# Optimization experiments

Measured on AMD Instinct MI355X. Metric: run time of the kernel, lower is better.

Reference implementation:

```python
import jax, jax.numpy as jnp
import numpy as np

B, L, D, H = 4, 1024, 1024, 16
HD = D // H            # head_dim = 64
MAX_LEN = 1024         # pos_max_len
SCALE = HD ** 0.5


def setup_inputs() -> dict:
    key = jax.random.key(0)
    ks = jax.random.split(key, 7)
    sd = 1.0 / np.sqrt(D)
    x = jax.random.normal(ks[0], (B, L, D), dtype=jnp.float32)
    Wq = jax.random.normal(ks[1], (D, D), dtype=jnp.float32) * sd
    Wk = jax.random.normal(ks[2], (D, D), dtype=jnp.float32) * sd
    Wv = jax.random.normal(ks[3], (D, D), dtype=jnp.float32) * sd
    Wo = jax.random.normal(ks[4], (D, D), dtype=jnp.float32) * sd
    # relative positional embedding tables [2*max_len+1, head_dim]
    pek = jax.random.normal(ks[5], (2 * MAX_LEN + 1, HD), dtype=jnp.float32) / np.sqrt(HD)
    pev = jax.random.normal(ks[6], (2 * MAX_LEN + 1, HD), dtype=jnp.float32) / np.sqrt(HD)
    return {"x": x, "Wq": Wq, "Wk": Wk, "Wv": Wv, "Wo": Wo, "pek": pek, "pev": pev}


def _rel_idx(seq_len):
    r = jnp.arange(seq_len)
    dist = r[None, :] - r[:, None]                 # k - q, [L, L]
    return jnp.clip(dist, -MAX_LEN, MAX_LEN) + MAX_LEN


def reference(x, Wq, Wk, Wv, Wo, pek, pev):
    b, s, _ = x.shape
    # projections (nn.Linear: x @ W.T), split heads -> [b, h, s, d]
    def proj(W):
        return (x @ W.T).reshape(b, s, H, HD).transpose(0, 2, 1, 3)
    Q, K, V = proj(Wq), proj(Wk), proj(Wv)

    scores = jnp.einsum('bhqd,bhkd->bhqk', Q, K) / SCALE
    idx = _rel_idx(s)                              # [s, s]
    rel_k = pek[idx]                               # [s, s, hd]
    scores = scores + jnp.einsum('bhqd,qkd->bhqk', Q, rel_k) / SCALE

    causal = jnp.tril(jnp.ones((s, s), dtype=bool))
    scores = jnp.where(causal[None, None], scores, -jnp.inf)
    attn = jax.nn.softmax(scores, axis=-1)         # [b, h, q, k]

    out = jnp.einsum('bhqk,bhkd->bhqd', attn, V)
    rel_v = pev[idx]                               # [s, s, hd]
    out = out + jnp.einsum('bhqk,qkd->bhqd', attn, rel_v)

    out = out.transpose(0, 2, 1, 3).reshape(b, s, D)
    return out @ Wo.T
```

## Files before the change

### kernel.cpp

```cpp
#include <hip/hip_runtime.h>
#include <hip/hip_bf16.h>

typedef __hip_bfloat16 bf16;
using bfv8 = __attribute__((ext_vector_type(8))) __bf16;
using f4_t = __attribute__((ext_vector_type(4))) float;

#define DEVI static __device__ __forceinline__

DEVI unsigned short f2bu(float f) {
    bf16 h = __float2bfloat16(f);
    return __builtin_bit_cast(unsigned short, h);
}
DEVI ushort4 f4_to_b4(float4 v) {
    ushort4 r;
    r.x = f2bu(v.x); r.y = f2bu(v.y); r.z = f2bu(v.z); r.w = f2bu(v.w);
    return r;
}
DEVI void gl2lds16(const void* g, void* l) {
    __builtin_amdgcn_global_load_lds((const __attribute__((address_space(1))) void*)g,
                                     (__attribute__((address_space(3))) void*)l, 16, 0, 0);
}

template<int N>
DEVI float row_ror(float x) {
    return __builtin_bit_cast(float,
        __builtin_amdgcn_update_dpp(0, __builtin_bit_cast(int, x), 0x120 | N, 0xF, 0xF, false));
}
DEVI float max16(float x) {
    x = fmaxf(x, row_ror<8>(x));
    x = fmaxf(x, row_ror<4>(x));
    x = fmaxf(x, row_ror<2>(x));
    x = fmaxf(x, row_ror<1>(x));
    return x;
}
DEVI float sum16(float x) {
    x += row_ror<8>(x);
    x += row_ror<4>(x);
    x += row_ror<2>(x);
    x += row_ror<1>(x);
    return x;
}

__global__ __launch_bounds__(256) void prep_cast(
    const float* __restrict__ x, const float* __restrict__ wq, const float* __restrict__ wk,
    const float* __restrict__ wv, const float* __restrict__ wo,
    bf16* __restrict__ xb, bf16* __restrict__ wqb, bf16* __restrict__ wkb,
    bf16* __restrict__ wvb, bf16* __restrict__ wob)
{
    size_t i = (size_t)blockIdx.x * 256 + threadIdx.x;
    const size_t X4 = 1u << 20, W4 = 1u << 18;
    const float* src; bf16* dst; size_t off;
    if (i < X4)              { src = x;  dst = xb;  off = i; }
    else if (i < X4 + W4)    { src = wq; dst = wqb; off = i - X4; }
    else if (i < X4 + 2*W4)  { src = wk; dst = wkb; off = i - X4 - W4; }
    else if (i < X4 + 3*W4)  { src = wv; dst = wvb; off = i - X4 - 2*W4; }
    else                     { src = wo; dst = wob; off = i - X4 - 3*W4; }
    float4 v = ((const float4*)src)[off];
    ((ushort4*)dst)[off] = f4_to_b4(v);
}

__global__ __launch_bounds__(256) void prep_blocks(
    const float* __restrict__ pek, const float* __restrict__ pev,
    bf16* __restrict__ pekBlk, bf16* __restrict__ pevBlk)
{
    __shared__ bf16 t[64][72];
    const int b = blockIdx.x;
    const int r = threadIdx.x >> 2, c0 = (threadIdx.x & 3) * 16;

    if (b < 17) {
        const float* src = pek + (size_t)(64 * b + 1 + r) * 64 + c0;
        bf16* dst = pekBlk + (size_t)b * 4096 + r * 64 + c0;
#pragma unroll
        for (int j = 0; j < 16; j += 4)
            *(ushort4*)(dst + j) = f4_to_b4(*(const float4*)(src + j));
    }
    {
        const float* src = pev + (size_t)(64 * b + 1 + r) * 64 + c0;
#pragma unroll
        for (int j = 0; j < 16; j++) t[r][c0 + j] = __float2bfloat16(src[j]);
        __syncthreads();
        bf16* dst = pevBlk + (size_t)b * 4096 + r * 64 + c0;
#pragma unroll
        for (int j = 0; j < 16; j++) dst[j] = t[c0 + j][r];
    }
}

__global__ __launch_bounds__(256, 2) void gemm_bt4(
    const bf16* __restrict__ A,
    const bf16* __restrict__ B0, const bf16* __restrict__ B1, const bf16* __restrict__ B2,
    bf16* __restrict__ outb, bf16* __restrict__ vtb, float* __restrict__ outf,
    int K, int mode)
{
    __shared__ __align__(16) bf16 smem[128 * 132];
    bf16* As = smem;
    bf16* Bs = smem + 128 * 64;
    bf16* Cb = smem;

    const int tid  = threadIdx.x;
    const int lane = tid & 63, wave = tid >> 6;
    const int quad = lane >> 4, l16 = lane & 15;
    const int wm = wave >> 1, wn = wave & 1;
    const int m0 = blockIdx.y * 128, n0 = blockIdx.x * 128;
    const int z = blockIdx.z;
    const bf16* Bm = (z == 0) ? B0 : (z == 1) ? B1 : B2;

    const int srow8 = lane >> 3;
    const int scg   = (lane & 7) ^ srow8;
    const int x8    = l16 & 7;

    f4_t zero = {0.f, 0.f, 0.f, 0.f};
    f4_t acc[4][4];
#pragma unroll
    for (int i = 0; i < 4; i++)
#pragma unroll
        for (int j = 0; j < 4; j++) acc[i][j] = zero;

    const bf16* Ag = A  + (size_t)(m0 + 32 * wave + srow8) * K + scg * 8;
    const bf16* Bg = Bm + (size_t)(n0 + 32 * wave + srow8) * K + scg * 8;

    for (int k0 = 0; k0 < K; k0 += 64) {
#pragma unroll
        for (int i = 0; i < 4; i++) {
            gl2lds16(Ag + (size_t)(8 * i) * K + k0, &As[(32 * wave + 8 * i) * 64]);
            gl2lds16(Bg + (size_t)(8 * i) * K + k0, &Bs[(32 * wave + 8 * i) * 64]);
        }
        __syncthreads();
#pragma unroll
        for (int ks = 0; ks < 2; ks++) {
            bfv8 af[4], bfr[4];
#pragma unroll
            for (int mt = 0; mt < 4; mt++)
                af[mt] = *(const bfv8*)&As[(wm * 64 + mt * 16 + l16) * 64 + ((ks * 4 + quad) ^ x8) * 8];
#pragma unroll
            for (int nt = 0; nt < 4; nt++)
                bfr[nt] = *(const bfv8*)&Bs[(wn * 64 + nt * 16 + l16) * 64 + ((ks * 4 + quad) ^ x8) * 8];
#pragma unroll
            for (int mt = 0; mt < 4; mt++)
#pragma unroll
                for (int nt = 0; nt < 4; nt++)
                    acc[mt][nt] = __builtin_amdgcn_mfma_f32_16x16x32_bf16(af[mt], bfr[nt], acc[mt][nt], 0, 0, 0);
        }
        __syncthreads();
    }

    if (mode == 1) {
#pragma unroll
        for (int mt = 0; mt < 4; mt++)
#pragma unroll
            for (int nt = 0; nt < 4; nt++)
#pragma unroll
                for (int r = 0; r < 4; r++) {
                    int m = m0 + wm * 64 + mt * 16 + quad * 4 + r;
                    int n = n0 + wn * 64 + nt * 16 + l16;
                    outf[(size_t)m * 1024 + n] = acc[mt][nt][r];
                }
        return;
    }

    const int b  = m0 >> 10, l0 = m0 & 1023, h0 = n0 >> 6;
    if (z < 2) {
#pragma unroll
        for (int mt = 0; mt < 4; mt++)
#pragma unroll
            for (int nt = 0; nt < 4; nt++)
#pragma unroll
                for (int r = 0; r < 4; r++) {
                    int mm = wm * 64 + mt * 16 + quad * 4 + r;
                    int nn = wn * 64 + nt * 16 + l16;
                    Cb[mm * 132 + nn] = __float2bfloat16(acc[mt][nt][r]);
                }
        __syncthreads();
        bf16* ob = outb + (size_t)z * (4 * 16 * 1024 * 64);
        const int hp = tid >> 7, lrow = tid & 127;
        bf16* dst = ob + ((size_t)((b * 16 + h0 + hp) * 1024) + l0 + lrow) * 64;
        const bf16* srcl = &Cb[lrow * 132 + hp * 64];
#pragma unroll
        for (int j = 0; j < 8; j++)
            *(int4*)(dst + 8 * j) = *(const int4*)(srcl + 8 * j);
    } else {
#pragma unroll
        for (int mt = 0; mt < 4; mt++)
#pragma unroll
            for (int nt = 0; nt < 4; nt++)
#pragma unroll
                for (int r = 0; r < 4; r++) {
                    int mm = wm * 64 + mt * 16 + quad * 4 + r;
                    int nn = wn * 64 + nt * 16 + l16;
                    Cb[nn * 132 + mm] = __float2bfloat16(acc[mt][nt][r]);
                }
        __syncthreads();
        const int ri = tid >> 1, c0 = (tid & 1) * 64;
        const int n = n0 + ri, h = n >> 6, hd = n & 63;
        bf16* dst = vtb + ((size_t)((b * 16 + h) * 64 + hd)) * 1024 + l0 + c0;
        const bf16* srcl = &Cb[ri * 132 + c0];
#pragma unroll
        for (int j = 0; j < 8; j++)
            *(int4*)(dst + 8 * j) = *(const int4*)(srcl + 8 * j);
    }
}

__global__ __launch_bounds__(256, 2) void attn_k(
    const bf16* __restrict__ Qb, const bf16* __restrict__ Kb, const bf16* __restrict__ Vtb,
    const bf16* __restrict__ pekBlk, const bf16* __restrict__ pevBlk, bf16* __restrict__ Ob)
{
    constexpr int ST = 104;
    __shared__ __align__(16) bf16 Ks[64 * 64];
    __shared__ __align__(16) bf16 Vs[64 * 64];
    __shared__ __align__(16) bf16 pekR[2 * 4096];
    __shared__ __align__(16) bf16 pevR[3 * 4096];
    __shared__ __align__(16) bf16 sU[4][16 * ST];
    __shared__ __align__(16) bf16 sP[4][16 * 72];

    const int tid  = threadIdx.x;
    const int lane = tid & 63, wave = tid >> 6;
    const int quad = lane >> 4, l16 = lane & 15;
    const int bh = blockIdx.x;
    const int g  = 15 - blockIdx.y;
    const int s  = 4 * g + wave;
    const int nkt = g + 1;

    bf16* myU = sU[wave];
    bf16* myP = sP[wave];

    const int srow8 = lane >> 3;
    const int scg   = (lane & 7) ^ srow8;
    const int x8    = l16 & 7;

    {
        int* p = (int*)myU;
#pragma unroll
        for (int i = 0; i < 13; i++) p[lane + 64 * i] = 0;
    }

    bfv8 qf[2];
    {
        const bf16* qp = Qb + ((size_t)bh * 1024 + 16 * s + l16) * 64 + quad * 8;
        qf[0] = *(const bfv8*)qp;
        qf[1] = *(const bfv8*)(qp + 32);
#pragma unroll
        for (int j = 0; j < 8; j++) {
            qf[0][j] = (__bf16)((float)qf[0][j] * 0.125f);
            qf[1][j] = (__bf16)((float)qf[1][j] * 0.125f);
        }
    }

    f4_t zero = {0.f, 0.f, 0.f, 0.f};
    f4_t o_acc[4];
    float m_i[4], l_i[4];
#pragma unroll
    for (int i = 0; i < 4; i++) { o_acc[i] = zero; m_i[i] = -1e30f; l_i[i] = 0.f; }

    const bf16* Kbh = Kb  + (size_t)bh * 1024 * 64;
    const bf16* Vbh = Vtb + (size_t)bh * 64 * 1024;
    const int B0 = 15 - g;

#pragma unroll
    for (int i = 0; i < 2; i++) {
        const int row = 8 * wave + 32 * i + srow8;
        gl2lds16(Kbh + (size_t)row * 64 + scg * 8, &Ks[(8 * wave + 32 * i) * 64]);
        gl2lds16(Vbh + (size_t)row * 1024 + scg * 8, &Vs[(8 * wave + 32 * i) * 64]);
    }
#pragma unroll
    for (int i2 = 0; i2 < 2; i2++) {
        const int slot = (B0 + i2) & 1;
#pragma unroll
        for (int i = 0; i < 2; i++) {
            const int row = 16 * wave + 8 * i + srow8;
            gl2lds16(pekBlk + (size_t)(B0 + i2) * 4096 + row * 64 + scg * 8,
                     &pekR[slot * 4096 + (16 * wave + 8 * i) * 64]);
        }
    }
#pragma unroll
    for (int i2 = 0; i2 < 3; i2++) {
        const int slot = (B0 + i2) % 3;
#pragma unroll
        for (int i = 0; i < 2; i++) {
            const int row = 16 * wave + 8 * i + srow8;
            gl2lds16(pevBlk + (size_t)(B0 + i2) * 4096 + row * 64 + scg * 8,
                     &pevR[slot * 4096 + (16 * wave + 8 * i) * 64]);
        }
    }
    __syncthreads();

    bfv8 stK[2], stV[2], stPk[2], stPv[2];

    for (int kt = 0; kt < nkt; kt++) {
        const int k0 = kt << 6;
        const int Bb = kt - g + 15;
        const int bm3 = Bb % 3;
        const bool pf = (kt + 1 < nkt);

        if (pf) {
            const int k0n = (kt + 1) << 6;
            const int bNew = Bb + 2, cNew = Bb + 3;
#pragma unroll
            for (int i = 0; i < 2; i++) {
                const int row = 8 * wave + 32 * i + srow8;
                stK[i] = *(const bfv8*)(Kbh + (size_t)(k0n + row) * 64 + scg * 8);
                stV[i] = *(const bfv8*)(Vbh + (size_t)row * 1024 + k0n + scg * 8);
            }
#pragma unroll
            for (int i = 0; i < 2; i++) {
                const int row = 16 * wave + 8 * i + srow8;
                stPk[i] = *(const bfv8*)(pekBlk + (size_t)bNew * 4096 + row * 64 + scg * 8);
                stPv[i] = *(const bfv8*)(pevBlk + (size_t)cNew * 4096 + row * 64 + scg * 8);
            }
        }

        f4_t s1[4], tt[5];
#pragma unroll
        for (int i = 0; i < 4; i++) s1[i] = zero;
#pragma unroll
        for (int i = 0; i < 5; i++) tt[i] = zero;
#pragma unroll
        for (int ks = 0; ks < 2; ks++) {
#pragma unroll
            for (int nt = 0; nt < 4; nt++) {
                bfv8 kf = *(const bfv8*)&Ks[(nt * 16 + l16) * 64 + ((ks * 4 + quad) ^ x8) * 8];
                s1[nt] = __builtin_amdgcn_mfma_f32_16x16x32_bf16(qf[ks], kf, s1[nt], 0, 0, 0);
            }
#pragma unroll
            for (int nt = 0; nt < 5; nt++) {
                const int off  = 48 - 16 * wave + 16 * nt;
                const int slot = (Bb + (off >> 6)) & 1;
                bfv8 pfr = *(const bfv8*)&pekR[slot * 4096 + ((off & 63) + l16) * 64
                                              + ((ks * 4 + quad) ^ x8) * 8];
                tt[nt] = __builtin_amdgcn_mfma_f32_16x16x32_bf16(qf[ks], pfr, tt[nt], 0, 0, 0);
            }
        }

        float sc[4][4];
#pragma unroll
        for (int r = 0; r < 4; r++) {
            int qq = quad * 4 + r;
            int t  = l16 + 15 - qq;
            int srcl = quad * 16 + (t & 15);
            bool lo = (t < 16);
            float rot[5];
#pragma unroll
            for (int j = 0; j < 5; j++) rot[j] = __shfl(tt[j][r], srcl, 64);
#pragma unroll
            for (int nt = 0; nt < 4; nt++) {
                float s2 = lo ? rot[nt] : rot[nt + 1];
                float v = s1[nt][r] + s2;
                int kk = nt * 16 + l16;
                if (k0 + kk > 16 * s + qq) v = -1e30f;
                sc[nt][r] = v;
            }
        }

        float alpha[4];
#pragma unroll
        for (int r = 0; r < 4; r++) {
            float mt = fmaxf(fmaxf(sc[0][r], sc[1][r]), fmaxf(sc[2][r], sc[3][r]));
            mt = max16(mt);
            float mnew = fmaxf(m_i[r], mt);
            alpha[r] = __expf(m_i[r] - mnew);
            m_i[r] = mnew;
        }
#pragma unroll
        for (int nt = 0; nt < 4; nt++)
#pragma unroll
            for (int r = 0; r < 4; r++)
                sc[nt][r] = __expf(sc[nt][r] - m_i[r]);
#pragma unroll
        for (int r = 0; r < 4; r++) {
            float rs = sum16(sc[0][r] + sc[1][r] + sc[2][r] + sc[3][r]);
            l_i[r] = l_i[r] * alpha[r] + rs;
#pragma unroll
            for (int nt = 0; nt < 4; nt++) o_acc[nt][r] *= alpha[r];
        }

#pragma unroll
        for (int nt = 0; nt < 4; nt++)
#pragma unroll
            for (int r = 0; r < 4; r++) {
                int qq = quad * 4 + r;
                int kk = nt * 16 + l16;
                bf16 pb = __float2bfloat16(sc[nt][r]);
                myP[qq * 72 + kk] = pb;
                myU[qq * ST + kk - qq + 15] = pb;
            }

#pragma unroll
        for (int ks = 0; ks < 2; ks++) {
            bfv8 pa = *(const bfv8*)&myP[l16 * 72 + ks * 32 + quad * 8];
#pragma unroll
            for (int nt = 0; nt < 4; nt++) {
                bfv8 vf = *(const bfv8*)&Vs[(nt * 16 + l16) * 64 + ((ks * 4 + quad) ^ x8) * 8];
                o_acc[nt] = __builtin_amdgcn_mfma_f32_16x16x32_bf16(pa, vf, o_acc[nt], 0, 0, 0);
            }
        }
#pragma unroll
        for (int ks = 0; ks < 3; ks++) {
            bfv8 ua = *(const bfv8*)&myU[l16 * ST + ks * 32 + quad * 8];
            const int off2 = 48 - 16 * wave + 32 * ks + 8 * quad;
            int slot2 = bm3 + (off2 >> 6);
            if (slot2 >= 3) slot2 -= 3;
            const int chunk = (((off2 & 63) >> 3) ^ x8);
#pragma unroll
            for (int nt = 0; nt < 4; nt++) {
                bfv8 pvf = *(const bfv8*)&pevR[slot2 * 4096 + (nt * 16 + l16) * 64 + chunk * 8];
                o_acc[nt] = __builtin_amdgcn_mfma_f32_16x16x32_bf16(ua, pvf, o_acc[nt], 0, 0, 0);
            }
        }
        __syncthreads();

        if (pf) {
            const int Bn = Bb + 1;
            const int slotK = (Bn + 1) & 1, slotV = (Bn + 2) % 3;
#pragma unroll
            for (int i = 0; i < 2; i++) {
                *(bfv8*)&Ks[(8 * wave + 32 * i) * 64 + lane * 8] = stK[i];
                *(bfv8*)&Vs[(8 * wave + 32 * i) * 64 + lane * 8] = stV[i];
            }
#pragma unroll
            for (int i = 0; i < 2; i++) {
                *(bfv8*)&pekR[slotK * 4096 + (16 * wave + 8 * i) * 64 + lane * 8] = stPk[i];
                *(bfv8*)&pevR[slotV * 4096 + (16 * wave + 8 * i) * 64 + lane * 8] = stPv[i];
            }
        }
        __syncthreads();
    }

    const int b = bh >> 4, h = bh & 15;
#pragma unroll
    for (int nt = 0; nt < 4; nt++)
#pragma unroll
        for (int r = 0; r < 4; r++) {
            int q = 16 * s + quad * 4 + r;
            int d = nt * 16 + l16;
            Ob[((size_t)(b * 1024 + q)) * 1024 + h * 64 + d] = __float2bfloat16(o_acc[nt][r] / l_i[r]);
        }
}

extern "C" void kernel_launch(void* const* d_in, const int* in_sizes, int n_in,
                              void* d_out, int out_size, void* d_ws, size_t ws_size,
                              hipStream_t stream) {
    const float* x   = (const float*)d_in[0];
    const float* Wq  = (const float*)d_in[1];
    const float* Wk  = (const float*)d_in[2];
    const float* Wv  = (const float*)d_in[3];
    const float* Wo  = (const float*)d_in[4];
    const float* pek = (const float*)d_in[5];
    const float* pev = (const float*)d_in[6];

    const size_t MB = 1u << 20;
    char* ws = (char*)d_ws;
    bf16* xb     = (bf16*)(ws + 0);
    bf16* Wqb    = (bf16*)(ws + 8  * MB);
    bf16* Wkb    = (bf16*)(ws + 10 * MB);
    bf16* Wvb    = (bf16*)(ws + 12 * MB);
    bf16* Wob    = (bf16*)(ws + 14 * MB);
    bf16* Qb     = (bf16*)(ws + 16 * MB);
    bf16* Kb     = (bf16*)(ws + 24 * MB);
    bf16* Vtb    = (bf16*)(ws + 32 * MB);
    bf16* pekBlk = (bf16*)(ws + 48 * MB);
    bf16* pevBlk = (bf16*)(ws + 48 * MB + 256*1024);
    bf16* Ao     = xb;

    prep_cast<<<dim3(8192), 256, 0, stream>>>(x, Wq, Wk, Wv, Wo, xb, Wqb, Wkb, Wvb, Wob);
    prep_blocks<<<dim3(18), 256, 0, stream>>>(pek, pev, pekBlk, pevBlk);
    gemm_bt4<<<dim3(8, 32, 3), 256, 0, stream>>>(xb, Wqb, Wkb, Wvb, Qb, Vtb, nullptr, 1024, 0);
    attn_k<<<dim3(64, 16), 256, 0, stream>>>(Qb, Kb, Vtb, pekBlk, pevBlk, Ao);
    gemm_bt4<<<dim3(8, 32, 1), 256, 0, stream>>>(Ao, Wob, nullptr, nullptr, nullptr, nullptr, (float*)d_out, 1024, 1);
}
```

Measured before the change: 206.3 us.

## Read pev fragments directly from global, drop pevR LDS staging, fuse prep kernels

Removes the triple-buffered pevR shared-memory ring and its prefetch/store, and instead loads the relative-value-embedding MFMA fragments directly from the transposed global pevBlk into registers each iteration. The P tile buffer is switched from padded rows to an XOR-swizzled layout, and the two prep kernels are merged into one launch. The aim is to cut LDS footprint and LDS traffic and save one launch, at the cost of more register pressure and global/L2 latency inside the inner loop.

After: 231.3 us. +12.1%, slower.

```diff
diff --git a/kernel.cpp b/kernel.cpp
--- a/kernel.cpp
+++ b/kernel.cpp
@@ -41,30 +41,29 @@
     return x;
 }
 
-__global__ __launch_bounds__(256) void prep_cast(
+__global__ __launch_bounds__(256) void prep_all(
     const float* __restrict__ x, const float* __restrict__ wq, const float* __restrict__ wk,
     const float* __restrict__ wv, const float* __restrict__ wo,
+    const float* __restrict__ pek, const float* __restrict__ pev,
     bf16* __restrict__ xb, bf16* __restrict__ wqb, bf16* __restrict__ wkb,
-    bf16* __restrict__ wvb, bf16* __restrict__ wob)
-{
-    size_t i = (size_t)blockIdx.x * 256 + threadIdx.x;
-    const size_t X4 = 1u << 20, W4 = 1u << 18;
-    const float* src; bf16* dst; size_t off;
-    if (i < X4)              { src = x;  dst = xb;  off = i; }
-    else if (i < X4 + W4)    { src = wq; dst = wqb; off = i - X4; }
-    else if (i < X4 + 2*W4)  { src = wk; dst = wkb; off = i - X4 - W4; }
-    else if (i < X4 + 3*W4)  { src = wv; dst = wvb; off = i - X4 - 2*W4; }
-    else                     { src = wo; dst = wob; off = i - X4 - 3*W4; }
-    float4 v = ((const float4*)src)[off];
-    ((ushort4*)dst)[off] = f4_to_b4(v);
-}
-
-__global__ __launch_bounds__(256) void prep_blocks(
-    const float* __restrict__ pek, const float* __restrict__ pev,
+    bf16* __restrict__ wvb, bf16* __restrict__ wob,
     bf16* __restrict__ pekBlk, bf16* __restrict__ pevBlk)
 {
     __shared__ bf16 t[64][72];
-    const int b = blockIdx.x;
+    if (blockIdx.x < 8192) {
+        size_t i = (size_t)blockIdx.x * 256 + threadIdx.x;
+        const size_t X4 = 1u << 20, W4 = 1u << 18;
+        const float* src; bf16* dst; size_t off;
+        if (i < X4)              { src = x;  dst = xb;  off = i; }
+        else if (i < X4 + W4)    { src = wq; dst = wqb; off = i - X4; }
+        else if (i < X4 + 2*W4)  { src = wk; dst = wkb; off = i - X4 - W4; }
+        else if (i < X4 + 3*W4)  { src = wv; dst = wvb; off = i - X4 - 2*W4; }
+        else                     { src = wo; dst = wob; off = i - X4 - 3*W4; }
+        float4 v = ((const float4*)src)[off];
+        ((ushort4*)dst)[off] = f4_to_b4(v);
+        return;
+    }
+    const int b = blockIdx.x - 8192;
     const int r = threadIdx.x >> 2, c0 = (threadIdx.x & 3) * 16;
 
     if (b < 17) {
@@ -207,9 +206,8 @@
     __shared__ __align__(16) bf16 Ks[64 * 64];
     __shared__ __align__(16) bf16 Vs[64 * 64];
     __shared__ __align__(16) bf16 pekR[2 * 4096];
-    __shared__ __align__(16) bf16 pevR[3 * 4096];
     __shared__ __align__(16) bf16 sU[4][16 * ST];
-    __shared__ __align__(16) bf16 sP[4][16 * 72];
+    __shared__ __align__(16) bf16 sP[4][16 * 64];
 
     const int tid  = threadIdx.x;
     const int lane = tid & 63, wave = tid >> 6;
@@ -270,29 +268,18 @@
                      &pekR[slot * 4096 + (16 * wave + 8 * i) * 64]);
         }
     }
-#pragma unroll
-    for (int i2 = 0; i2 < 3; i2++) {
-        const int slot = (B0 + i2) % 3;
-#pragma unroll
-        for (int i = 0; i < 2; i++) {
-            const int row = 16 * wave + 8 * i + srow8;
-            gl2lds16(pevBlk + (size_t)(B0 + i2) * 4096 + row * 64 + scg * 8,
-                     &pevR[slot * 4096 + (16 * wave + 8 * i) * 64]);
-        }
-    }
     __syncthreads();
 
-    bfv8 stK[2], stV[2], stPk[2], stPv[2];
+    bfv8 stK[2], stV[2], stPk[2];
 
     for (int kt = 0; kt < nkt; kt++) {
         const int k0 = kt << 6;
         const int Bb = kt - g + 15;
-        const int bm3 = Bb % 3;
         const bool pf = (kt + 1 < nkt);
 
         if (pf) {
             const int k0n = (kt + 1) << 6;
-            const int bNew = Bb + 2, cNew = Bb + 3;
+            const int bNew = Bb + 2;
 #pragma unroll
             for (int i = 0; i < 2; i++) {
                 const int row = 8 * wave + 32 * i + srow8;
@@ -303,7 +290,6 @@
             for (int i = 0; i < 2; i++) {
                 const int row = 16 * wave + 8 * i + srow8;
                 stPk[i] = *(const bfv8*)(pekBlk + (size_t)bNew * 4096 + row * 64 + scg * 8);
-                stPv[i] = *(const bfv8*)(pevBlk + (size_t)cNew * 4096 + row * 64 + scg * 8);
             }
         }
 
@@ -371,6 +357,22 @@
             for (int nt = 0; nt < 4; nt++) o_acc[nt][r] *= alpha[r];
         }
 
+        bfv8 pvfA[4], pvfB[4], pvfC[4];
+        {
+            const int t0a = Bb * 64 + 48 - 16 * wave + 8 * quad;
+            const bf16* pvWa = pevBlk + (size_t)(t0a >> 6) * 4096 + (t0a & 63);
+            const int t0b = t0a + 32;
+            const bf16* pvWb = pevBlk + (size_t)(t0b >> 6) * 4096 + (t0b & 63);
+            const int t0c = t0a + 64;
+            const bf16* pvWc = pevBlk + (size_t)(t0c >> 6) * 4096 + (t0c & 63);
+#pragma unroll
+            for (int nt = 0; nt < 4; nt++) {
+                pvfA[nt] = *(const bfv8*)(pvWa + (size_t)(nt * 16 + l16) * 64);
+                pvfB[nt] = *(const bfv8*)(pvWb + (size_t)(nt * 16 + l16) * 64);
+                pvfC[nt] = *(const bfv8*)(pvWc + (size_t)(nt * 16 + l16) * 64);
+            }
+        }
+
 #pragma unroll
         for (int nt = 0; nt < 4; nt++)
 #pragma unroll
@@ -378,47 +380,46 @@
                 int qq = quad * 4 + r;
                 int kk = nt * 16 + l16;
                 bf16 pb = __float2bfloat16(sc[nt][r]);
-                myP[qq * 72 + kk] = pb;
+                myP[qq * 64 + (((kk >> 3) ^ (qq & 7)) << 3) + (kk & 7)] = pb;
                 myU[qq * ST + kk - qq + 15] = pb;
             }
 
 #pragma unroll
         for (int ks = 0; ks < 2; ks++) {
-            bfv8 pa = *(const bfv8*)&myP[l16 * 72 + ks * 32 + quad * 8];
+            bfv8 pa = *(const bfv8*)&myP[l16 * 64 + (((ks * 4 + quad) ^ x8) << 3)];
 #pragma unroll
             for (int nt = 0; nt < 4; nt++) {
                 bfv8 vf = *(const bfv8*)&Vs[(nt * 16 + l16) * 64 + ((ks * 4 + quad) ^ x8) * 8];
                 o_acc[nt] = __builtin_amdgcn_mfma_f32_16x16x32_bf16(pa, vf, o_acc[nt], 0, 0, 0);
             }
         }
-#pragma unroll
-        for (int ks = 0; ks < 3; ks++) {
-            bfv8 ua = *(const bfv8*)&myU[l16 * ST + ks * 32 + quad * 8];
-            const int off2 = 48 - 16 * wave + 32 * ks + 8 * quad;
-            int slot2 = bm3 + (off2 >> 6);
-            if (slot2 >= 3) slot2 -= 3;
-            const int chunk = (((off2 & 63) >> 3) ^ x8);
-#pragma unroll
-            for (int nt = 0; nt < 4; nt++) {
-                bfv8 pvf = *(const bfv8*)&pevR[slot2 * 4096 + (nt * 16 + l16) * 64 + chunk * 8];
-                o_acc[nt] = __builtin_amdgcn_mfma_f32_16x16x32_bf16(ua, pvf, o_acc[nt], 0, 0, 0);
-            }
+        {
+            bfv8 ua0 = *(const bfv8*)&myU[l16 * ST + 0 * 32 + quad * 8];
+#pragma unroll
+            for (int nt = 0; nt < 4; nt++)
+                o_acc[nt] = __builtin_amdgcn_mfma_f32_16x16x32_bf16(ua0, pvfA[nt], o_acc[nt], 0, 0, 0);
+            bfv8 ua1 = *(const bfv8*)&myU[l16 * ST + 1 * 32 + quad * 8];
+#pragma unroll
+            for (int nt = 0; nt < 4; nt++)
+                o_acc[nt] = __builtin_amdgcn_mfma_f32_16x16x32_bf16(ua1, pvfB[nt], o_acc[nt], 0, 0, 0);
+            bfv8 ua2 = *(const bfv8*)&myU[l16 * ST + 2 * 32 + quad * 8];
+#pragma unroll
+            for (int nt = 0; nt < 4; nt++)
+                o_acc[nt] = __builtin_amdgcn_mfma_f32_16x16x32_bf16(ua2, pvfC[nt], o_acc[nt], 0, 0, 0);
         }
         __syncthreads();
 
         if (pf) {
             const int Bn = Bb + 1;
-            const int slotK = (Bn + 1) & 1, slotV = (Bn + 2) % 3;
+            const int slotK = (Bn + 1) & 1;
 #pragma unroll
             for (int i = 0; i < 2; i++) {
                 *(bfv8*)&Ks[(8 * wave + 32 * i) * 64 + lane * 8] = stK[i];
                 *(bfv8*)&Vs[(8 * wave + 32 * i) * 64 + lane * 8] = stV[i];
             }
 #pragma unroll
-            for (int i = 0; i < 2; i++) {
+            for (int i = 0; i < 2; i++)
                 *(bfv8*)&pekR[slotK * 4096 + (16 * wave + 8 * i) * 64 + lane * 8] = stPk[i];
-                *(bfv8*)&pevR[slotV * 4096 + (16 * wave + 8 * i) * 64 + lane * 8] = stPv[i];
-            }
         }
         __syncthreads();
     }
@@ -459,8 +460,8 @@
     bf16* pevBlk = (bf16*)(ws + 48 * MB + 256*1024);
     bf16* Ao     = xb;
 
-    prep_cast<<<dim3(8192), 256, 0, stream>>>(x, Wq, Wk, Wv, Wo, xb, Wqb, Wkb, Wvb, Wob);
-    prep_blocks<<<dim3(18), 256, 0, stream>>>(pek, pev, pekBlk, pevBlk);
+    prep_all<<<dim3(8210), 256, 0, stream>>>(x, Wq, Wk, Wv, Wo, pek, pev,
+                                             xb, Wqb, Wkb, Wvb, Wob, pekBlk, pevBlk);
     gemm_bt4<<<dim3(8, 32, 3), 256, 0, stream>>>(xb, Wqb, Wkb, Wvb, Qb, Vtb, nullptr, 1024, 0);
     attn_k<<<dim3(64, 16), 256, 0, stream>>>(Qb, Kb, Vtb, pekBlk, pevBlk, Ao);
     gemm_bt4<<<dim3(8, 32, 1), 256, 0, stream>>>(Ao, Wob, nullptr, nullptr, nullptr, nullptr, (float*)d_out, 1024, 1);
```
